# Kernel optimization log

Measured on AMD Instinct MI355X. Metric: run time of the kernel, lower is better.

## Reference

```python
import jax, jax.numpy as jnp
import numpy as np

N, G, E, H, OUT, MAX_N = 131072, 256, 384, 6, 256, 1024
DH = E // H  # 64


def _make_sizes():
    # variable-length segments summing exactly to N, each in [1, MAX_N]
    rng = np.random.default_rng(0)
    raw = rng.integers(128, 896, G).astype(np.int64)
    diff = int(N - raw.sum())
    q, r = divmod(diff, G)
    sizes = raw + q
    sizes[:r] += 1
    assert sizes.sum() == N and sizes.min() >= 1 and sizes.max() <= MAX_N
    return sizes


def setup_inputs() -> dict:
    key = jax.random.key(0)
    ks = jax.random.split(key, 8)
    s = 1.0 / np.sqrt(E)
    return {
        "node_feat": jax.random.normal(ks[0], (N, E), jnp.float32),
        "sizes": jnp.asarray(_make_sizes(), jnp.int32),
        "query": jax.random.normal(ks[1], (E,), jnp.float32),
        "Wq": jax.random.normal(ks[2], (E, E), jnp.float32) * s,
        "bq": jnp.zeros((E,), jnp.float32),
        "Wk": jax.random.normal(ks[3], (E, E), jnp.float32) * s,
        "bk": jnp.zeros((E,), jnp.float32),
        "Wv": jax.random.normal(ks[4], (E, E), jnp.float32) * s,
        "bv": jnp.zeros((E,), jnp.float32),
        "Wo": jax.random.normal(ks[5], (E, E), jnp.float32) * s,
        "bo": jnp.zeros((E,), jnp.float32),
        "Wp": jax.random.normal(ks[6], (OUT, E), jnp.float32) * s,
        "bp": jnp.zeros((OUT,), jnp.float32),
    }


def reference(node_feat, sizes, query, Wq, bq, Wk, bk, Wv, bv, Wo, bo, Wp, bp):
    # segment offsets and padded gather indices
    offsets = jnp.cumsum(sizes) - sizes                      # [G]
    pos = jnp.arange(MAX_N)
    idx = jnp.clip(offsets[:, None] + pos[None, :], 0, N - 1)  # [G, MAX_N]
    mask = pos[None, :] < sizes[:, None]                     # [G, MAX_N]

    # project K/V on the flat node table (one big GEMM), then gather into padded form
    k_flat = node_feat @ Wk.T + bk                           # [N, E]
    v_flat = node_feat @ Wv.T + bv
    k = k_flat[idx].reshape(G, MAX_N, H, DH)
    v = v_flat[idx].reshape(G, MAX_N, H, DH)

    # single shared query token, pre-scaled (PyTorch MHA scales q by 1/sqrt(head_dim))
    q = ((query @ Wq.T + bq) * (1.0 / np.sqrt(DH))).reshape(H, DH)

    scores = jnp.einsum('hd,gnhd->ghn', q, k)                # [G, H, MAX_N]
    scores = jnp.where(mask[:, None, :], scores, -1e30)
    attn = jax.nn.softmax(scores, axis=-1)
    pooled = jnp.einsum('ghn,gnhd->ghd', attn, v).reshape(G, E)

    out = pooled @ Wo.T + bo                                 # MHA out_proj
    return out @ Wp.T + bp                                   # final proj  [G, OUT]
```

## Files before the change

kernel.cpp:

```cpp
#include <hip/hip_runtime.h>
#include <math.h>

#define NN 131072
#define G  256
#define E  384
#define H  6
#define DH 64
#define OUTD 256
#define MAXN 1024

#define CHK 128
#define SLOTS 8
#define PART_STRIDE 2316

#define WS_QK   0
#define WS_C    2304
#define WS_OFF  2432
#define WS_QV   2944
#define WS_WL   3328
#define WS_M    5376
#define WS_PART 5632
#define WS_WVT  (WS_PART + G*SLOTS*PART_STRIDE)
#define WS_WOT  (WS_WVT + E*E)
#define WS_WPT  (WS_WOT + E*E)

__global__ __launch_bounds__(256) void k0a_scan_qv(
    const int* __restrict__ sizes, const float* __restrict__ query,
    const float* __restrict__ Wq, const float* __restrict__ bq,
    float* __restrict__ wsf) {
  const int tid = threadIdx.x;
  if (blockIdx.x == 0) {
    __shared__ int s_scan[G];
    __shared__ int s_scan2[G];
    const int sz = sizes[tid];
    s_scan[tid] = sz;
    const int nch = (sz + CHK - 1) >> 7;
    s_scan2[tid] = nch;
    __syncthreads();
    for (int d = 1; d < G; d <<= 1) {
      int t = (tid >= d) ? s_scan[tid - d] : 0;
      int t2 = (tid >= d) ? s_scan2[tid - d] : 0;
      __syncthreads();
      s_scan[tid] += t;
      s_scan2[tid] += t2;
      __syncthreads();
    }
    int* offs = (int*)(wsf + WS_OFF);
    offs[tid] = s_scan[tid] - sz;
    int* wl = (int*)(wsf + WS_WL);
    const int pos = s_scan2[tid] - nch;
    for (int s = 0; s < nch; s++) wl[pos + s] = (tid << 3) | s;
    if (tid == G - 1) ((int*)(wsf + WS_M))[0] = s_scan2[G - 1];
  } else {
    const int lane = tid & 63;
    const int i = (blockIdx.x - 1) * 4 + (tid >> 6);
    float a = 0.f;
#pragma unroll
    for (int j = 0; j < 6; j++)
      a += Wq[(size_t)i * E + j * 64 + lane] * query[j * 64 + lane];
#pragma unroll
    for (int mm = 1; mm < 64; mm <<= 1) a += __shfl_xor(a, mm, 64);
    if (lane == 0) wsf[WS_QV + i] = 0.125f * (a + bq[i]);
  }
}

__global__ __launch_bounds__(256) void k0b_qk(
    const float* __restrict__ Wk, const float* __restrict__ bk,
    float* __restrict__ wsf) {
  __shared__ float qv_s[64];
  __shared__ float ps[256];
  const int h = blockIdx.x / 6, ec = blockIdx.x % 6;
  const int tid = threadIdx.x;
  if (tid < 64) qv_s[tid] = wsf[WS_QV + h * 64 + tid];
  __syncthreads();
  const int el = tid & 63, dq = tid >> 6;
  float a = 0.f;
#pragma unroll 4
  for (int d = dq * 16; d < dq * 16 + 16; d++)
    a += qv_s[d] * Wk[(size_t)(h * 64 + d) * E + ec * 64 + el];
  ps[tid] = a;
  __syncthreads();
  if (tid < 64)
    wsf[WS_QK + h * E + ec * 64 + tid] =
        ps[tid] + ps[64 + tid] + ps[128 + tid] + ps[192 + tid];
  if (ec == 0 && tid < 64) {
    float p = qv_s[tid] * bk[h * 64 + tid];
#pragma unroll
    for (int mm = 1; mm < 64; mm <<= 1) p += __shfl_xor(p, mm, 64);
    if (tid == 0) wsf[WS_C + h] = p;
  }
}

__global__ __launch_bounds__(256) void k0t_transpose(
    const float* __restrict__ Wv, const float* __restrict__ Wo,
    const float* __restrict__ Wp, float* __restrict__ wsf) {
  __shared__ float s[64][65];
  const int b = blockIdx.x;
  const float* src;
  float* dst;
  int R, tr, tc;
  if (b < 36)      { src = Wv; dst = wsf + WS_WVT; R = 384; tr = b / 6;        tc = b % 6; }
  else if (b < 72) { src = Wo; dst = wsf + WS_WOT; R = 384; tr = (b - 36) / 6; tc = (b - 36) % 6; }
  else             { src = Wp; dst = wsf + WS_WPT; R = 256; tr = (b - 72) / 6; tc = (b - 72) % 6; }
  const int r0 = tr * 64, c0 = tc * 64;
#pragma unroll
  for (int k = 0; k < 16; k++) {
    int idx = k * 256 + threadIdx.x;
    int r = idx >> 6, cc = idx & 63;
    s[r][cc] = src[(size_t)(r0 + r) * E + c0 + cc];
  }
  __syncthreads();
#pragma unroll
  for (int k = 0; k < 16; k++) {
    int idx = k * 256 + threadIdx.x;
    int cc = idx >> 6, r = idx & 63;
    dst[(size_t)(c0 + cc) * R + r0 + r] = s[r][cc];
  }
}

#define PB 136
__global__ __launch_bounds__(256) void k12_fused(
    const float* __restrict__ x, const int* __restrict__ sizes,
    float* __restrict__ wsf) {
  __shared__ float u_mem[4608];
  __shared__ float pbuf[H * PB];
  __shared__ float c_s[8];
  const int M = ((const int*)(wsf + WS_M))[0];
  if ((int)blockIdx.x >= M) return;
  const int item = ((const int*)(wsf + WS_WL))[blockIdx.x];
  const int g = item >> 3, s = item & 7;
  const int Ng = sizes[g];
  const int rem = Ng - s * CHK;
  const int clen = rem < CHK ? rem : CHK;
  const int n0 = ((const int*)(wsf + WS_OFF))[g] + s * CHK;
  const int tid = threadIdx.x;

  float* qk_l = u_mem;
  for (int idx = tid; idx < 2304; idx += 256) {
    int sub = idx / 288, r3 = idx % 288;
    int h = r3 / 48, r2 = r3 % 48, j = r2 >> 2, r = r2 & 3;
    qk_l[sub * 292 + h * 48 + j * 4 + r] =
        wsf[WS_QK + h * E + (j * 8 + sub) * 4 + r];
  }
  if (tid < 8) c_s[tid] = (tid < 6) ? wsf[WS_C + tid] : 0.f;
  __syncthreads();

  const int lane = tid & 63, w = tid >> 6;
  const int sub = lane & 7, nod = lane >> 3;
  const float4* x4 = (const float4*)x;
  {
    const int base = w * 32;
    float acc[4][6];
#pragma unroll
    for (int o = 0; o < 4; o++)
#pragma unroll
      for (int h = 0; h < 6; h++) acc[o][h] = 0.f;
#pragma unroll 4
    for (int j = 0; j < 12; j++) {
      float4 qk4[6];
#pragma unroll
      for (int h = 0; h < 6; h++)
        qk4[h] = *(const float4*)&qk_l[sub * 292 + h * 48 + j * 4];
      float4 xv[4];
#pragma unroll
      for (int o = 0; o < 4; o++) {
        int nn = base + o * 8 + nod;
        nn = nn < clen ? nn : clen - 1;
        xv[o] = x4[(size_t)(n0 + nn) * 96 + j * 8 + sub];
      }
#pragma unroll
      for (int o = 0; o < 4; o++)
#pragma unroll
        for (int h = 0; h < 6; h++)
          acc[o][h] += qk4[h].x * xv[o].x + qk4[h].y * xv[o].y
                     + qk4[h].z * xv[o].z + qk4[h].w * xv[o].w;
    }
#pragma unroll
    for (int o = 0; o < 4; o++) {
#pragma unroll
      for (int h = 0; h < 6; h++) {
        acc[o][h] += __shfl_xor(acc[o][h], 1, 64);
        acc[o][h] += __shfl_xor(acc[o][h], 2, 64);
        acc[o][h] += __shfl_xor(acc[o][h], 4, 64);
      }
      float v = acc[o][0];
#pragma unroll
      for (int h = 1; h < 6; h++) v = (sub == h) ? acc[o][h] : v;
      if (sub < 6) {
        int nn = base + o * 8 + nod;
        pbuf[sub * PB + nn] = (nn < clen) ? v + c_s[sub] : -1.0e30f;
      }
    }
  }
  __syncthreads();

  float* pslot = wsf + WS_PART + (size_t)blockIdx.x * PART_STRIDE;
  for (int h = w; h < 6; h += 4) {
    float v0 = pbuf[h * PB + lane], v1 = pbuf[h * PB + 64 + lane];
    float m = fmaxf(v0, v1);
#pragma unroll
    for (int mm = 1; mm < 64; mm <<= 1) m = fmaxf(m, __shfl_xor(m, mm, 64));
    float e0 = __expf(v0 - m), e1 = __expf(v1 - m);
    pbuf[h * PB + lane] = e0;
    pbuf[h * PB + 64 + lane] = e1;
    float l = e0 + e1;
#pragma unroll
    for (int mm = 1; mm < 64; mm <<= 1) l += __shfl_xor(l, mm, 64);
    if (lane == 0) { pslot[2304 + h] = m; pslot[2310 + h] = l; }
  }
  __syncthreads();

  float* psum = u_mem;
  if (tid < 192) {
    const int f4 = tid % 96, np = tid / 96;
    float acc[6][4];
#pragma unroll
    for (int h = 0; h < 6; h++)
#pragma unroll
      for (int c = 0; c < 4; c++) acc[h][c] = 0.f;
#pragma unroll 2
    for (int n = 0; n < 64; n += 4) {
      float4 xv[4];
#pragma unroll
      for (int k = 0; k < 4; k++) {
        int nn = np * 64 + n + k;
        nn = nn < clen ? nn : clen - 1;
        xv[k] = x4[(size_t)(n0 + nn) * 96 + f4];
      }
#pragma unroll
      for (int h = 0; h < 6; h++) {
        const float4 p = *(const float4*)&pbuf[h * PB + np * 64 + n];
#pragma unroll
        for (int c = 0; c < 4; c++) {
          const float* xc = (const float*)&xv[0];
        }
        acc[h][0] += p.x * xv[0].x + p.y * xv[1].x + p.z * xv[2].x + p.w * xv[3].x;
        acc[h][1] += p.x * xv[0].y + p.y * xv[1].y + p.z * xv[2].y + p.w * xv[3].y;
        acc[h][2] += p.x * xv[0].z + p.y * xv[1].z + p.z * xv[2].z + p.w * xv[3].z;
        acc[h][3] += p.x * xv[0].w + p.y * xv[1].w + p.z * xv[2].w + p.w * xv[3].w;
      }
    }
#pragma unroll
    for (int h = 0; h < 6; h++)
      *(float4*)&psum[(np * 6 + h) * E + f4 * 4] =
          make_float4(acc[h][0], acc[h][1], acc[h][2], acc[h][3]);
  }
  __syncthreads();
  for (int idx = tid; idx < 2304; idx += 256)
    pslot[idx] = psum[idx] + psum[2304 + idx];
}

__global__ __launch_bounds__(768) void k3_group(
    const float* __restrict__ wsf, const int* __restrict__ sizes,
    const float* __restrict__ bv, const float* __restrict__ bo,
    const float* __restrict__ bp, float* __restrict__ out) {
  __shared__ float xb[H * E];
  __shared__ float pooled[E];
  __shared__ float om[E];
  __shared__ float ps[768];
  __shared__ float wgt[SLOTS][H];
  __shared__ float linv[H];
  __shared__ int base_s;
  const int tid = threadIdx.x;
  const int g = blockIdx.x;
  const int nch = (sizes[g] + CHK - 1) >> 7;
  if (tid == 0) {
    int b = 0;
    for (int gg = 0; gg < g; gg++) b += (sizes[gg] + CHK - 1) >> 7;
    base_s = b;
  }
  __syncthreads();
  const float* pg = wsf + WS_PART + (size_t)base_s * PART_STRIDE;
  const float* wvt = wsf + WS_WVT;
  const float* wot = wsf + WS_WOT;
  const float* wpt = wsf + WS_WPT;

  if (tid < H) {
    float m = -3.0e38f;
    for (int s = 0; s < nch; s++)
      m = fmaxf(m, pg[(size_t)s * PART_STRIDE + 2304 + tid]);
    float L = 0.f;
    for (int s = 0; s < nch; s++) {
      float wv_ = __expf(pg[(size_t)s * PART_STRIDE + 2304 + tid] - m);
      wgt[s][tid] = wv_;
      L += pg[(size_t)s * PART_STRIDE + 2310 + tid] * wv_;
    }
    linv[tid] = 1.f / L;
  }
  __syncthreads();
  for (int idx = tid; idx < H * E; idx += 768) {
    int h = idx / E;
    float a = 0.f;
    for (int s = 0; s < nch; s++) a += pg[(size_t)s * PART_STRIDE + idx] * wgt[s][h];
    xb[idx] = a * linv[h];
  }
  __syncthreads();

  {
    const int i = tid % 384, ks = tid / 384;
    const float* xh = xb + (i >> 6) * E + ks * 192;
    const float* wp_ = wvt + (size_t)(ks * 192) * E + i;
    float a0 = 0.f, a1 = 0.f, a2 = 0.f, a3 = 0.f;
#pragma unroll 4
    for (int e = 0; e < 192; e += 4) {
      a0 += wp_[(size_t)(e + 0) * E] * xh[e + 0];
      a1 += wp_[(size_t)(e + 1) * E] * xh[e + 1];
      a2 += wp_[(size_t)(e + 2) * E] * xh[e + 2];
      a3 += wp_[(size_t)(e + 3) * E] * xh[e + 3];
    }
    ps[tid] = (a0 + a1) + (a2 + a3);
  }
  __syncthreads();
  if (tid < 384) pooled[tid] = ps[tid] + ps[384 + tid] + bv[tid];
  __syncthreads();

  {
    const int i = tid % 384, ks = tid / 384;
    const float* xh = pooled + ks * 192;
    const float* wp_ = wot + (size_t)(ks * 192) * E + i;
    float a0 = 0.f, a1 = 0.f, a2 = 0.f, a3 = 0.f;
#pragma unroll 4
    for (int e = 0; e < 192; e += 4) {
      a0 += wp_[(size_t)(e + 0) * E] * xh[e + 0];
      a1 += wp_[(size_t)(e + 1) * E] * xh[e + 1];
      a2 += wp_[(size_t)(e + 2) * E] * xh[e + 2];
      a3 += wp_[(size_t)(e + 3) * E] * xh[e + 3];
    }
    ps[tid] = (a0 + a1) + (a2 + a3);
  }
  __syncthreads();
  if (tid < 384) om[tid] = ps[tid] + ps[384 + tid] + bo[tid];
  __syncthreads();

  {
    const int o = tid % 256, ks = tid / 256;
    const float* xh = om + ks * 128;
    const float* wp_ = wpt + (size_t)(ks * 128) * OUTD + o;
    float a0 = 0.f, a1 = 0.f, a2 = 0.f, a3 = 0.f;
#pragma unroll 4
    for (int e = 0; e < 128; e += 4) {
      a0 += wp_[(size_t)(e + 0) * OUTD] * xh[e + 0];
      a1 += wp_[(size_t)(e + 1) * OUTD] * xh[e + 1];
      a2 += wp_[(size_t)(e + 2) * OUTD] * xh[e + 2];
      a3 += wp_[(size_t)(e + 3) * OUTD] * xh[e + 3];
    }
    ps[tid] = (a0 + a1) + (a2 + a3);
  }
  __syncthreads();
  if (tid < 256)
    out[(size_t)g * OUTD + tid] = ps[tid] + ps[256 + tid] + ps[512 + tid] + bp[tid];
}

extern "C" void kernel_launch(void* const* d_in, const int* in_sizes, int n_in,
                              void* d_out, int out_size, void* d_ws, size_t ws_size,
                              hipStream_t stream) {
  const float* x     = (const float*)d_in[0];
  const int*   sizes = (const int*)d_in[1];
  const float* query = (const float*)d_in[2];
  const float* Wq    = (const float*)d_in[3];
  const float* bq    = (const float*)d_in[4];
  const float* Wk    = (const float*)d_in[5];
  const float* bk    = (const float*)d_in[6];
  const float* Wv    = (const float*)d_in[7];
  const float* bv    = (const float*)d_in[8];
  const float* Wo    = (const float*)d_in[9];
  const float* bo    = (const float*)d_in[10];
  const float* Wp    = (const float*)d_in[11];
  const float* bp    = (const float*)d_in[12];
  float* wsf = (float*)d_ws;
  float* out = (float*)d_out;

  hipLaunchKernelGGL(k0a_scan_qv, dim3(97), dim3(256), 0, stream,
                     sizes, query, Wq, bq, wsf);
  hipLaunchKernelGGL(k0b_qk, dim3(36), dim3(256), 0, stream, Wk, bk, wsf);
  hipLaunchKernelGGL(k0t_transpose, dim3(96), dim3(256), 0, stream,
                     Wv, Wo, Wp, wsf);
  hipLaunchKernelGGL(k12_fused, dim3(G * SLOTS), dim3(256), 0, stream,
                     x, sizes, wsf);
  hipLaunchKernelGGL(k3_group, dim3(G), dim3(768), 0, stream,
                     wsf, sizes, bv, bo, bp, out);
}
```

Before: 373.3 us.

## Stage node tiles in LDS via direct global-to-LDS loads with online softmax

The fused score/pool kernel now copies 32-node tiles of x into shared memory with global_load_lds, then computes scores and the weighted sum from LDS. A running max and sum (online softmax) replace the old two-pass read of x from global memory. The block grows to 384 threads, and k3 reads a precomputed chunk offset instead of serially summing one in each block. The aim is to read x from global memory once instead of twice. In exchange there are more barriers per tile, only 2 of 6 waves do the scoring, and the larger LDS footprint may lower occupancy.

```diff
diff --git a/kernel.cpp b/kernel.cpp
--- a/kernel.cpp
+++ b/kernel.cpp
@@ -11,6 +11,7 @@
 
 #define CHK 128
 #define SLOTS 8
+#define TILE 32
 #define PART_STRIDE 2316
 
 #define WS_QK   0
@@ -19,10 +20,17 @@
 #define WS_QV   2944
 #define WS_WL   3328
 #define WS_M    5376
-#define WS_PART 5632
+#define WS_CS   5632
+#define WS_PART 6144
 #define WS_WVT  (WS_PART + G*SLOTS*PART_STRIDE)
 #define WS_WOT  (WS_WVT + E*E)
 #define WS_WPT  (WS_WOT + E*E)
+
+__device__ __forceinline__ void gload16(const float* g, float* l) {
+  __builtin_amdgcn_global_load_lds(
+      (const __attribute__((address_space(1))) unsigned int*)g,
+      (__attribute__((address_space(3))) unsigned int*)l, 16, 0, 0);
+}
 
 __global__ __launch_bounds__(256) void k0a_scan_qv(
     const int* __restrict__ sizes, const float* __restrict__ query,
@@ -45,10 +53,10 @@
       s_scan2[tid] += t2;
       __syncthreads();
     }
-    int* offs = (int*)(wsf + WS_OFF);
-    offs[tid] = s_scan[tid] - sz;
+    ((int*)(wsf + WS_OFF))[tid] = s_scan[tid] - sz;
+    const int pos = s_scan2[tid] - nch;
+    ((int*)(wsf + WS_CS))[tid] = pos;
     int* wl = (int*)(wsf + WS_WL);
-    const int pos = s_scan2[tid] - nch;
     for (int s = 0; s < nch; s++) wl[pos + s] = (tid << 3) | s;
     if (tid == G - 1) ((int*)(wsf + WS_M))[0] = s_scan2[G - 1];
   } else {
@@ -118,13 +126,14 @@
   }
 }
 
-#define PB 136
-__global__ __launch_bounds__(256) void k12_fused(
+__global__ __launch_bounds__(384, 3) void k12_fused(
     const float* __restrict__ x, const int* __restrict__ sizes,
     float* __restrict__ wsf) {
-  __shared__ float u_mem[4608];
-  __shared__ float pbuf[H * PB];
+  __shared__ float xt[TILE * 384];
+  __shared__ float qk_l[8 * 292];
+  __shared__ float pe[TILE * 8];
   __shared__ float c_s[8];
+  __shared__ float s_m[8], s_l[8], s_alpha[8];
   const int M = ((const int*)(wsf + WS_M))[0];
   if ((int)blockIdx.x >= M) return;
   const int item = ((const int*)(wsf + WS_WL))[blockIdx.x];
@@ -133,121 +142,162 @@
   const int rem = Ng - s * CHK;
   const int clen = rem < CHK ? rem : CHK;
   const int n0 = ((const int*)(wsf + WS_OFF))[g] + s * CHK;
+  const int nt = (clen + TILE - 1) >> 5;
   const int tid = threadIdx.x;
-
-  float* qk_l = u_mem;
-  for (int idx = tid; idx < 2304; idx += 256) {
+  const int lane = tid & 63, w = tid >> 6;
+
+  for (int idx = tid; idx < 2304; idx += 384) {
     int sub = idx / 288, r3 = idx % 288;
     int h = r3 / 48, r2 = r3 % 48, j = r2 >> 2, r = r2 & 3;
     qk_l[sub * 292 + h * 48 + j * 4 + r] =
         wsf[WS_QK + h * E + (j * 8 + sub) * 4 + r];
   }
-  if (tid < 8) c_s[tid] = (tid < 6) ? wsf[WS_C + tid] : 0.f;
-  __syncthreads();
-
-  const int lane = tid & 63, w = tid >> 6;
+  if (tid < 8) {
+    c_s[tid] = (tid < 6) ? wsf[WS_C + tid] : 0.f;
+    s_m[tid] = -3.0e38f;
+    s_l[tid] = 0.f;
+  }
+
+  const int f4 = tid % 96, np = tid / 96;
+  float acc[6][4];
+#pragma unroll
+  for (int h = 0; h < 6; h++)
+#pragma unroll
+    for (int c = 0; c < 4; c++) acc[h][c] = 0.f;
+
+  const size_t xcap = (size_t)NN * E - 4;
   const int sub = lane & 7, nod = lane >> 3;
-  const float4* x4 = (const float4*)x;
-  {
-    const int base = w * 32;
-    float acc[4][6];
-#pragma unroll
-    for (int o = 0; o < 4; o++)
-#pragma unroll
-      for (int h = 0; h < 6; h++) acc[o][h] = 0.f;
+
+  for (int t = 0; t < nt; t++) {
+    {
+      const size_t tb = (size_t)(n0 + t * TILE) * E;
+      int nbytes = (clen - t * TILE) * (E * 4);
+      if (nbytes > TILE * E * 4) nbytes = TILE * E * 4;
+      const int nseg = (nbytes + 1023) >> 10;
+#pragma unroll
+      for (int it = 0; it < 8; it++) {
+        const int seg = it * 6 + w;
+        if (seg < nseg) {
+          size_t gi = tb + seg * 256 + lane * 4;
+          if (gi > xcap) gi = xcap;
+          gload16(x + gi, &xt[seg * 256 + lane * 4]);
+        }
+      }
+    }
+    __syncthreads();
+
+    if (w < 2) {
+      float a2[2][6];
+#pragma unroll
+      for (int o = 0; o < 2; o++)
+#pragma unroll
+        for (int h = 0; h < 6; h++) a2[o][h] = 0.f;
 #pragma unroll 4
-    for (int j = 0; j < 12; j++) {
-      float4 qk4[6];
+      for (int j = 0; j < 12; j++) {
+        float4 qk4[6];
+#pragma unroll
+        for (int h = 0; h < 6; h++)
+          qk4[h] = *(const float4*)&qk_l[sub * 292 + h * 48 + j * 4];
+        float4 xv[2];
+#pragma unroll
+        for (int o = 0; o < 2; o++)
+          xv[o] = *(const float4*)&xt[(w * 16 + o * 8 + nod) * 384 +
+                                      (j * 8 + sub) * 4];
+#pragma unroll
+        for (int o = 0; o < 2; o++)
+#pragma unroll
+          for (int h = 0; h < 6; h++)
+            a2[o][h] += qk4[h].x * xv[o].x + qk4[h].y * xv[o].y
+                      + qk4[h].z * xv[o].z + qk4[h].w * xv[o].w;
+      }
+#pragma unroll
+      for (int o = 0; o < 2; o++) {
+#pragma unroll
+        for (int h = 0; h < 6; h++) {
+          a2[o][h] += __shfl_xor(a2[o][h], 1, 64);
+          a2[o][h] += __shfl_xor(a2[o][h], 2, 64);
+          a2[o][h] += __shfl_xor(a2[o][h], 4, 64);
+        }
+        float v = a2[o][0];
+#pragma unroll
+        for (int h = 1; h < 6; h++) v = (sub == h) ? a2[o][h] : v;
+        const int nl = w * 16 + o * 8 + nod;
+        if (sub < 6)
+          pe[nl * 8 + sub] =
+              (t * TILE + nl < clen) ? v + c_s[sub] : -1.0e30f;
+      }
+    }
+    __syncthreads();
+
+    {
+      const int n = lane & 31;
+      const float v = pe[n * 8 + w];
+      float mt = v;
+#pragma unroll
+      for (int mm = 1; mm < 64; mm <<= 1) mt = fmaxf(mt, __shfl_xor(mt, mm, 64));
+      const float mold = s_m[w];
+      const float mnew = fmaxf(mold, mt);
+      const float e = __expf(v - mnew);
+      float lt = (lane < 32) ? e : 0.f;
+#pragma unroll
+      for (int mm = 1; mm < 64; mm <<= 1) lt += __shfl_xor(lt, mm, 64);
+      if (lane < 32) pe[n * 8 + w] = e;
+      if (lane == 0) {
+        const float alpha = __expf(mold - mnew);
+        s_alpha[w] = alpha;
+        s_l[w] = s_l[w] * alpha + lt;
+        s_m[w] = mnew;
+      }
+    }
+    __syncthreads();
+
+    {
+      float al[6];
+#pragma unroll
+      for (int h = 0; h < 6; h++) al[h] = s_alpha[h];
 #pragma unroll
       for (int h = 0; h < 6; h++)
-        qk4[h] = *(const float4*)&qk_l[sub * 292 + h * 48 + j * 4];
-      float4 xv[4];
-#pragma unroll
-      for (int o = 0; o < 4; o++) {
-        int nn = base + o * 8 + nod;
-        nn = nn < clen ? nn : clen - 1;
-        xv[o] = x4[(size_t)(n0 + nn) * 96 + j * 8 + sub];
+#pragma unroll
+        for (int c = 0; c < 4; c++) acc[h][c] *= al[h];
+#pragma unroll
+      for (int n8 = 0; n8 < 8; n8++) {
+        const int n = np * 8 + n8;
+        const float4 xv = *(const float4*)&xt[n * 384 + f4 * 4];
+        const float4 pA = *(const float4*)&pe[n * 8];
+        const float2 pB = *(const float2*)&pe[n * 8 + 4];
+        acc[0][0] += pA.x * xv.x; acc[0][1] += pA.x * xv.y;
+        acc[0][2] += pA.x * xv.z; acc[0][3] += pA.x * xv.w;
+        acc[1][0] += pA.y * xv.x; acc[1][1] += pA.y * xv.y;
+        acc[1][2] += pA.y * xv.z; acc[1][3] += pA.y * xv.w;
+        acc[2][0] += pA.z * xv.x; acc[2][1] += pA.z * xv.y;
+        acc[2][2] += pA.z * xv.z; acc[2][3] += pA.z * xv.w;
+        acc[3][0] += pA.w * xv.x; acc[3][1] += pA.w * xv.y;
+        acc[3][2] += pA.w * xv.z; acc[3][3] += pA.w * xv.w;
+        acc[4][0] += pB.x * xv.x; acc[4][1] += pB.x * xv.y;
+        acc[4][2] += pB.x * xv.z; acc[4][3] += pB.x * xv.w;
+        acc[5][0] += pB.y * xv.x; acc[5][1] += pB.y * xv.y;
+        acc[5][2] += pB.y * xv.z; acc[5][3] += pB.y * xv.w;
       }
-#pragma unroll
-      for (int o = 0; o < 4; o++)
-#pragma unroll
-        for (int h = 0; h < 6; h++)
-          acc[o][h] += qk4[h].x * xv[o].x + qk4[h].y * xv[o].y
-                     + qk4[h].z * xv[o].z + qk4[h].w * xv[o].w;
-    }
-#pragma unroll
-    for (int o = 0; o < 4; o++) {
-#pragma unroll
-      for (int h = 0; h < 6; h++) {
-        acc[o][h] += __shfl_xor(acc[o][h], 1, 64);
-        acc[o][h] += __shfl_xor(acc[o][h], 2, 64);
-        acc[o][h] += __shfl_xor(acc[o][h], 4, 64);
-      }
-      float v = acc[o][0];
-#pragma unroll
-      for (int h = 1; h < 6; h++) v = (sub == h) ? acc[o][h] : v;
-      if (sub < 6) {
-        int nn = base + o * 8 + nod;
-        pbuf[sub * PB + nn] = (nn < clen) ? v + c_s[sub] : -1.0e30f;
-      }
-    }
-  }
-  __syncthreads();
-
+    }
+    __syncthreads();
+  }
+
+#pragma unroll
+  for (int h = 0; h < 6; h++)
+    *(float4*)&xt[(np * 6 + h) * 384 + f4 * 4] =
+        make_float4(acc[h][0], acc[h][1], acc[h][2], acc[h][3]);
+  __syncthreads();
   float* pslot = wsf + WS_PART + (size_t)blockIdx.x * PART_STRIDE;
-  for (int h = w; h < 6; h += 4) {
-    float v0 = pbuf[h * PB + lane], v1 = pbuf[h * PB + 64 + lane];
-    float m = fmaxf(v0, v1);
-#pragma unroll
-    for (int mm = 1; mm < 64; mm <<= 1) m = fmaxf(m, __shfl_xor(m, mm, 64));
-    float e0 = __expf(v0 - m), e1 = __expf(v1 - m);
-    pbuf[h * PB + lane] = e0;
-    pbuf[h * PB + 64 + lane] = e1;
-    float l = e0 + e1;
-#pragma unroll
-    for (int mm = 1; mm < 64; mm <<= 1) l += __shfl_xor(l, mm, 64);
-    if (lane == 0) { pslot[2304 + h] = m; pslot[2310 + h] = l; }
-  }
-  __syncthreads();
-
-  float* psum = u_mem;
-  if (tid < 192) {
-    const int f4 = tid % 96, np = tid / 96;
-    float acc[6][4];
-#pragma unroll
-    for (int h = 0; h < 6; h++)
-#pragma unroll
-      for (int c = 0; c < 4; c++) acc[h][c] = 0.f;
-#pragma unroll 2
-    for (int n = 0; n < 64; n += 4) {
-      float4 xv[4];
-#pragma unroll
-      for (int k = 0; k < 4; k++) {
-        int nn = np * 64 + n + k;
-        nn = nn < clen ? nn : clen - 1;
-        xv[k] = x4[(size_t)(n0 + nn) * 96 + f4];
-      }
-#pragma unroll
-      for (int h = 0; h < 6; h++) {
-        const float4 p = *(const float4*)&pbuf[h * PB + np * 64 + n];
-#pragma unroll
-        for (int c = 0; c < 4; c++) {
-          const float* xc = (const float*)&xv[0];
-        }
-        acc[h][0] += p.x * xv[0].x + p.y * xv[1].x + p.z * xv[2].x + p.w * xv[3].x;
-        acc[h][1] += p.x * xv[0].y + p.y * xv[1].y + p.z * xv[2].y + p.w * xv[3].y;
-        acc[h][2] += p.x * xv[0].z + p.y * xv[1].z + p.z * xv[2].z + p.w * xv[3].z;
-        acc[h][3] += p.x * xv[0].w + p.y * xv[1].w + p.z * xv[2].w + p.w * xv[3].w;
-      }
-    }
-#pragma unroll
-    for (int h = 0; h < 6; h++)
-      *(float4*)&psum[(np * 6 + h) * E + f4 * 4] =
-          make_float4(acc[h][0], acc[h][1], acc[h][2], acc[h][3]);
-  }
-  __syncthreads();
-  for (int idx = tid; idx < 2304; idx += 256)
-    pslot[idx] = psum[idx] + psum[2304 + idx];
+#pragma unroll
+  for (int h = 0; h < 6; h++) {
+    float a = xt[(0 * 6 + h) * 384 + tid] + xt[(1 * 6 + h) * 384 + tid]
+            + xt[(2 * 6 + h) * 384 + tid] + xt[(3 * 6 + h) * 384 + tid];
+    pslot[h * E + tid] = a;
+  }
+  if (tid < 6) {
+    pslot[2304 + tid] = s_m[tid];
+    pslot[2310 + tid] = s_l[tid];
+  }
 }
 
 __global__ __launch_bounds__(768) void k3_group(
@@ -260,16 +310,10 @@
   __shared__ float ps[768];
   __shared__ float wgt[SLOTS][H];
   __shared__ float linv[H];
-  __shared__ int base_s;
   const int tid = threadIdx.x;
   const int g = blockIdx.x;
   const int nch = (sizes[g] + CHK - 1) >> 7;
-  if (tid == 0) {
-    int b = 0;
-    for (int gg = 0; gg < g; gg++) b += (sizes[gg] + CHK - 1) >> 7;
-    base_s = b;
-  }
-  __syncthreads();
+  const int base_s = ((const int*)(wsf + WS_CS))[g];
   const float* pg = wsf + WS_PART + (size_t)base_s * PART_STRIDE;
   const float* wvt = wsf + WS_WVT;
   const float* wot = wsf + WS_WOT;
@@ -375,7 +419,7 @@
   hipLaunchKernelGGL(k0b_qk, dim3(36), dim3(256), 0, stream, Wk, bk, wsf);
   hipLaunchKernelGGL(k0t_transpose, dim3(96), dim3(256), 0, stream,
                      Wv, Wo, Wp, wsf);
-  hipLaunchKernelGGL(k12_fused, dim3(G * SLOTS), dim3(256), 0, stream,
+  hipLaunchKernelGGL(k12_fused, dim3(G * SLOTS), dim3(384), 0, stream,
                      x, sizes, wsf);
   hipLaunchKernelGGL(k3_group, dim3(G), dim3(768), 0, stream,
                      wsf, sizes, bv, bo, bp, out);
```

New measurement: 400.2 us. 1.07x slower.

## Assign one 32-node chunk per warp and drop intra-block syncs in fused attention

Applied to the files above, without the earlier changes.

The segment chunk size drops from 128 to 32 nodes, and each wavefront now handles one chunk on its own: scores, local softmax and the weighted sum of x, with no block-wide barriers and no cross-wave shared-memory reduction. The scan kernel now also stores per-group chunk-start offsets, so the group kernel no longer recomputes the prefix serially in one thread. The group kernel also stages per-slot max and sum values in shared memory before merging. The trade-off is about four times more partial-sum records written to and read back from global memory, plus a longer cross-chunk merge in the group kernel.

```diff
diff --git a/kernel.cpp b/kernel.cpp
--- a/kernel.cpp
+++ b/kernel.cpp
@@ -9,8 +9,8 @@
 #define OUTD 256
 #define MAXN 1024
 
-#define CHK 128
-#define SLOTS 8
+#define CHK 32
+#define SLOTS 32
 #define PART_STRIDE 2316
 
 #define WS_QK   0
@@ -18,8 +18,9 @@
 #define WS_OFF  2432
 #define WS_QV   2944
 #define WS_WL   3328
-#define WS_M    5376
-#define WS_PART 5632
+#define WS_M    11520
+#define WS_CS   11776
+#define WS_PART 12288
 #define WS_WVT  (WS_PART + G*SLOTS*PART_STRIDE)
 #define WS_WOT  (WS_WVT + E*E)
 #define WS_WPT  (WS_WOT + E*E)
@@ -34,7 +35,7 @@
     __shared__ int s_scan2[G];
     const int sz = sizes[tid];
     s_scan[tid] = sz;
-    const int nch = (sz + CHK - 1) >> 7;
+    const int nch = (sz + CHK - 1) >> 5;
     s_scan2[tid] = nch;
     __syncthreads();
     for (int d = 1; d < G; d <<= 1) {
@@ -45,11 +46,11 @@
       s_scan2[tid] += t2;
       __syncthreads();
     }
-    int* offs = (int*)(wsf + WS_OFF);
-    offs[tid] = s_scan[tid] - sz;
+    ((int*)(wsf + WS_OFF))[tid] = s_scan[tid] - sz;
+    const int pos = s_scan2[tid] - nch;
+    ((int*)(wsf + WS_CS))[tid] = pos;
     int* wl = (int*)(wsf + WS_WL);
-    const int pos = s_scan2[tid] - nch;
-    for (int s = 0; s < nch; s++) wl[pos + s] = (tid << 3) | s;
+    for (int s = 0; s < nch; s++) wl[pos + s] = (tid << 5) | s;
     if (tid == G - 1) ((int*)(wsf + WS_M))[0] = s_scan2[G - 1];
   } else {
     const int lane = tid & 63;
@@ -118,24 +119,13 @@
   }
 }
 
-#define PB 136
 __global__ __launch_bounds__(256) void k12_fused(
     const float* __restrict__ x, const int* __restrict__ sizes,
     float* __restrict__ wsf) {
-  __shared__ float u_mem[4608];
-  __shared__ float pbuf[H * PB];
+  __shared__ float qk_l[8 * 292];
   __shared__ float c_s[8];
-  const int M = ((const int*)(wsf + WS_M))[0];
-  if ((int)blockIdx.x >= M) return;
-  const int item = ((const int*)(wsf + WS_WL))[blockIdx.x];
-  const int g = item >> 3, s = item & 7;
-  const int Ng = sizes[g];
-  const int rem = Ng - s * CHK;
-  const int clen = rem < CHK ? rem : CHK;
-  const int n0 = ((const int*)(wsf + WS_OFF))[g] + s * CHK;
+  __shared__ float pe2[4][CHK * 8];
   const int tid = threadIdx.x;
-
-  float* qk_l = u_mem;
   for (int idx = tid; idx < 2304; idx += 256) {
     int sub = idx / 288, r3 = idx % 288;
     int h = r3 / 48, r2 = r3 % 48, j = r2 >> 2, r = r2 & 3;
@@ -146,10 +136,21 @@
   __syncthreads();
 
   const int lane = tid & 63, w = tid >> 6;
+  const int gw = blockIdx.x * 4 + w;
+  const int M = ((const int*)(wsf + WS_M))[0];
+  if (gw >= M) return;
+  const int item = ((const int*)(wsf + WS_WL))[gw];
+  const int g = item >> 5, s = item & 31;
+  const int Ng = sizes[g];
+  const int rem = Ng - s * CHK;
+  const int clen = rem < CHK ? rem : CHK;
+  const int n0 = ((const int*)(wsf + WS_OFF))[g] + s * CHK;
+  float* pe = pe2[w];
+  float* pslot = wsf + WS_PART + (size_t)gw * PART_STRIDE;
   const int sub = lane & 7, nod = lane >> 3;
   const float4* x4 = (const float4*)x;
-  {
-    const int base = w * 32;
+
+  {
     float acc[4][6];
 #pragma unroll
     for (int o = 0; o < 4; o++)
@@ -164,7 +165,7 @@
       float4 xv[4];
 #pragma unroll
       for (int o = 0; o < 4; o++) {
-        int nn = base + o * 8 + nod;
+        int nn = o * 8 + nod;
         nn = nn < clen ? nn : clen - 1;
         xv[o] = x4[(size_t)(n0 + nn) * 96 + j * 8 + sub];
       }
@@ -186,68 +187,79 @@
       float v = acc[o][0];
 #pragma unroll
       for (int h = 1; h < 6; h++) v = (sub == h) ? acc[o][h] : v;
-      if (sub < 6) {
-        int nn = base + o * 8 + nod;
-        pbuf[sub * PB + nn] = (nn < clen) ? v + c_s[sub] : -1.0e30f;
+      const int nl = o * 8 + nod;
+      if (sub < 6)
+        pe[nl * 8 + sub] = (nl < clen) ? v + c_s[sub] : -1.0e30f;
+    }
+  }
+
+  if (lane < 32) {
+    const float4 sA = *(const float4*)&pe[lane * 8];
+    const float2 sB = *(const float2*)&pe[lane * 8 + 4];
+    float sc[6] = {sA.x, sA.y, sA.z, sA.w, sB.x, sB.y};
+    float mh[6], lh[6], eh[6];
+#pragma unroll
+    for (int h = 0; h < 6; h++) {
+      float t = sc[h];
+#pragma unroll
+      for (int mm = 1; mm < 32; mm <<= 1) t = fmaxf(t, __shfl_xor(t, mm, 32));
+      mh[h] = t;
+      eh[h] = __expf(sc[h] - t);
+    }
+#pragma unroll
+    for (int h = 0; h < 6; h++) {
+      float t = eh[h];
+#pragma unroll
+      for (int mm = 1; mm < 32; mm <<= 1) t += __shfl_xor(t, mm, 32);
+      lh[h] = t;
+    }
+    *(float4*)&pe[lane * 8] = make_float4(eh[0], eh[1], eh[2], eh[3]);
+    *(float2*)&pe[lane * 8 + 4] = make_float2(eh[4], eh[5]);
+    if (lane < 6) {
+      float vm = mh[0], vl = lh[0];
+#pragma unroll
+      for (int h = 1; h < 6; h++) {
+        vm = (lane == h) ? mh[h] : vm;
+        vl = (lane == h) ? lh[h] : vl;
       }
-    }
-  }
-  __syncthreads();
-
-  float* pslot = wsf + WS_PART + (size_t)blockIdx.x * PART_STRIDE;
-  for (int h = w; h < 6; h += 4) {
-    float v0 = pbuf[h * PB + lane], v1 = pbuf[h * PB + 64 + lane];
-    float m = fmaxf(v0, v1);
-#pragma unroll
-    for (int mm = 1; mm < 64; mm <<= 1) m = fmaxf(m, __shfl_xor(m, mm, 64));
-    float e0 = __expf(v0 - m), e1 = __expf(v1 - m);
-    pbuf[h * PB + lane] = e0;
-    pbuf[h * PB + 64 + lane] = e1;
-    float l = e0 + e1;
-#pragma unroll
-    for (int mm = 1; mm < 64; mm <<= 1) l += __shfl_xor(l, mm, 64);
-    if (lane == 0) { pslot[2304 + h] = m; pslot[2310 + h] = l; }
-  }
-  __syncthreads();
-
-  float* psum = u_mem;
-  if (tid < 192) {
-    const int f4 = tid % 96, np = tid / 96;
-    float acc[6][4];
+      pslot[2304 + lane] = vm;
+      pslot[2310 + lane] = vl;
+    }
+  }
+
+  {
+    float accA[6][4], accB[6][4];
 #pragma unroll
     for (int h = 0; h < 6; h++)
 #pragma unroll
-      for (int c = 0; c < 4; c++) acc[h][c] = 0.f;
+      for (int c = 0; c < 4; c++) { accA[h][c] = 0.f; accB[h][c] = 0.f; }
+    const float4* xr = x4 + (size_t)n0 * 96;
+    const int colB = 64 + (lane & 31);
 #pragma unroll 2
-    for (int n = 0; n < 64; n += 4) {
-      float4 xv[4];
-#pragma unroll
-      for (int k = 0; k < 4; k++) {
-        int nn = np * 64 + n + k;
-        nn = nn < clen ? nn : clen - 1;
-        xv[k] = x4[(size_t)(n0 + nn) * 96 + f4];
+    for (int n = 0; n < clen; n++) {
+      const float4 xA = xr[n * 96 + lane];
+      const float4 xB = xr[n * 96 + colB];
+      const float4 pA = *(const float4*)&pe[n * 8];
+      const float2 pB = *(const float2*)&pe[n * 8 + 4];
+      const float ph[6] = {pA.x, pA.y, pA.z, pA.w, pB.x, pB.y};
+#pragma unroll
+      for (int h = 0; h < 6; h++) {
+        accA[h][0] += ph[h] * xA.x; accA[h][1] += ph[h] * xA.y;
+        accA[h][2] += ph[h] * xA.z; accA[h][3] += ph[h] * xA.w;
+        accB[h][0] += ph[h] * xB.x; accB[h][1] += ph[h] * xB.y;
+        accB[h][2] += ph[h] * xB.z; accB[h][3] += ph[h] * xB.w;
       }
-#pragma unroll
-      for (int h = 0; h < 6; h++) {
-        const float4 p = *(const float4*)&pbuf[h * PB + np * 64 + n];
-#pragma unroll
-        for (int c = 0; c < 4; c++) {
-          const float* xc = (const float*)&xv[0];
-        }
-        acc[h][0] += p.x * xv[0].x + p.y * xv[1].x + p.z * xv[2].x + p.w * xv[3].x;
-        acc[h][1] += p.x * xv[0].y + p.y * xv[1].y + p.z * xv[2].y + p.w * xv[3].y;
-        acc[h][2] += p.x * xv[0].z + p.y * xv[1].z + p.z * xv[2].z + p.w * xv[3].z;
-        acc[h][3] += p.x * xv[0].w + p.y * xv[1].w + p.z * xv[2].w + p.w * xv[3].w;
-      }
     }
 #pragma unroll
     for (int h = 0; h < 6; h++)
-      *(float4*)&psum[(np * 6 + h) * E + f4 * 4] =
-          make_float4(acc[h][0], acc[h][1], acc[h][2], acc[h][3]);
-  }
-  __syncthreads();
-  for (int idx = tid; idx < 2304; idx += 256)
-    pslot[idx] = psum[idx] + psum[2304 + idx];
+      *(float4*)&pslot[h * E + lane * 4] =
+          make_float4(accA[h][0], accA[h][1], accA[h][2], accA[h][3]);
+    if (lane < 32)
+#pragma unroll
+      for (int h = 0; h < 6; h++)
+        *(float4*)&pslot[h * E + 256 + lane * 4] =
+            make_float4(accB[h][0], accB[h][1], accB[h][2], accB[h][3]);
+  }
 }
 
 __global__ __launch_bounds__(768) void k3_group(
@@ -258,32 +270,33 @@
   __shared__ float pooled[E];
   __shared__ float om[E];
   __shared__ float ps[768];
-  __shared__ float wgt[SLOTS][H];
+  __shared__ float msh[SLOTS][H], lsh[SLOTS][H], wgt[SLOTS][H];
   __shared__ float linv[H];
-  __shared__ int base_s;
   const int tid = threadIdx.x;
   const int g = blockIdx.x;
-  const int nch = (sizes[g] + CHK - 1) >> 7;
-  if (tid == 0) {
-    int b = 0;
-    for (int gg = 0; gg < g; gg++) b += (sizes[gg] + CHK - 1) >> 7;
-    base_s = b;
-  }
-  __syncthreads();
+  const int nch = (sizes[g] + CHK - 1) >> 5;
+  const int base_s = ((const int*)(wsf + WS_CS))[g];
   const float* pg = wsf + WS_PART + (size_t)base_s * PART_STRIDE;
   const float* wvt = wsf + WS_WVT;
   const float* wot = wsf + WS_WOT;
   const float* wpt = wsf + WS_WPT;
 
+  if (tid < SLOTS * H) {
+    const int s2 = tid / H, h2 = tid % H;
+    if (s2 < nch) {
+      msh[s2][h2] = pg[(size_t)s2 * PART_STRIDE + 2304 + h2];
+      lsh[s2][h2] = pg[(size_t)s2 * PART_STRIDE + 2310 + h2];
+    }
+  }
+  __syncthreads();
   if (tid < H) {
     float m = -3.0e38f;
-    for (int s = 0; s < nch; s++)
-      m = fmaxf(m, pg[(size_t)s * PART_STRIDE + 2304 + tid]);
+    for (int s = 0; s < nch; s++) m = fmaxf(m, msh[s][tid]);
     float L = 0.f;
     for (int s = 0; s < nch; s++) {
-      float wv_ = __expf(pg[(size_t)s * PART_STRIDE + 2304 + tid] - m);
+      float wv_ = __expf(msh[s][tid] - m);
       wgt[s][tid] = wv_;
-      L += pg[(size_t)s * PART_STRIDE + 2310 + tid] * wv_;
+      L += lsh[s][tid] * wv_;
     }
     linv[tid] = 1.f / L;
   }
@@ -375,7 +388,7 @@
   hipLaunchKernelGGL(k0b_qk, dim3(36), dim3(256), 0, stream, Wk, bk, wsf);
   hipLaunchKernelGGL(k0t_transpose, dim3(96), dim3(256), 0, stream,
                      Wv, Wo, Wp, wsf);
-  hipLaunchKernelGGL(k12_fused, dim3(G * SLOTS), dim3(256), 0, stream,
+  hipLaunchKernelGGL(k12_fused, dim3(1088), dim3(256), 0, stream,
                      x, sizes, wsf);
   hipLaunchKernelGGL(k3_group, dim3(G), dim3(768), 0, stream,
                      wsf, sizes, bv, bo, bp, out);
```

Result: no change. 375.2 us (+0.5%).
